# Optimization experiments

Hardware: AMD Instinct MI355X
Metric: run time of the kernel (lower is better)

## Reference

```python
import jax, jax.numpy as jnp
import numpy as np

N, D, H = 4096, 1024, 8
DH = D // H
EPS = 1e-5


def layer_norm(x, g, b):
    mu = jnp.mean(x, axis=-1, keepdims=True)
    var = jnp.mean(jnp.square(x - mu), axis=-1, keepdims=True)
    return (x - mu) * jax.lax.rsqrt(var + EPS) * g + b


def setup_inputs() -> dict:
    key = jax.random.key(0)
    ks = jax.random.split(key, 12)
    s = 0.02
    inp = {
        "x": jax.random.normal(ks[0], (N, D), dtype=jnp.float32),
        "adj": (jax.random.uniform(ks[1], (N, N)) < 0.01).astype(jnp.float32),
        "Wq": jax.random.normal(ks[2], (D, D), dtype=jnp.float32) * s,
        "Wk": jax.random.normal(ks[3], (D, D), dtype=jnp.float32) * s,
        "Wv": jax.random.normal(ks[4], (D, D), dtype=jnp.float32) * s,
        "Wo_w": jax.random.normal(ks[5], (D, D), dtype=jnp.float32) * s,
        "Wo_b": jnp.zeros((D,), dtype=jnp.float32),
        "adj_bias": jnp.full((H,), 1.0, dtype=jnp.float32),
        "ln1_g": jnp.ones((D,), dtype=jnp.float32),
        "ln1_b": jnp.zeros((D,), dtype=jnp.float32),
        "ffn_ln_g": jnp.ones((D,), dtype=jnp.float32),
        "ffn_ln_b": jnp.zeros((D,), dtype=jnp.float32),
        "ffn_w1": jax.random.normal(ks[6], (D, 2 * D), dtype=jnp.float32) * s,
        "ffn_b1": jnp.zeros((2 * D,), dtype=jnp.float32),
        "ffn_w2": jax.random.normal(ks[7], (2 * D, D), dtype=jnp.float32) * s,
        "ffn_b2": jnp.zeros((D,), dtype=jnp.float32),
    }
    return inp


def reference(x, adj, Wq, Wk, Wv, Wo_w, Wo_b, adj_bias, ln1_g, ln1_b,
              ffn_ln_g, ffn_ln_b, ffn_w1, ffn_b1, ffn_w2, ffn_b2):
    scale = DH ** -0.5
    Q = (x @ Wq).reshape(N, H, DH)
    K = (x @ Wk).reshape(N, H, DH)
    V = (x @ Wv).reshape(N, H, DH)
    # attn[i,h,j] = <Q_i, K_j> * scale + beta_h * adj[i,j]
    attn = jnp.einsum('bhd,nhd->bhn', Q, K) * scale
    attn = attn + adj_bias[None, :, None] * adj[:, None, :]
    attn = jax.nn.softmax(attn, axis=-1)  # dropout in eval mode -> identity
    out = jnp.einsum('bhn,nhd->bhd', attn, V).reshape(N, D)
    out = out @ Wo_w + Wo_b
    h = layer_norm(x + out, ln1_g, ln1_b)
    f = layer_norm(h, ffn_ln_g, ffn_ln_b)
    f = jax.nn.gelu(f @ ffn_w1 + ffn_b1, approximate=False) @ ffn_w2 + ffn_b2
    return h + f
```

## Files before the change

### kernel.cpp

```cpp
#include <hip/hip_runtime.h>
#include <hip/hip_bf16.h>
#include <cstdint>
#include <cstddef>

typedef __hip_bfloat16 bf16;
typedef __attribute__((ext_vector_type(8))) short short8;
typedef __attribute__((ext_vector_type(4))) short short4v;
typedef __attribute__((ext_vector_type(4))) float floatx4;
typedef unsigned long long u64;

#define DEVI static __device__ __forceinline__

DEVI void load_lds16(const void* g, void* l) {
  __builtin_amdgcn_global_load_lds((const __attribute__((address_space(1))) unsigned int*)g,
                                   (__attribute__((address_space(3))) unsigned int*)l, 16, 0, 0);
}
DEVI short8 ld8(const bf16* p) { return *(const short8*)p; }
DEVI floatx4 mfma16(short8 a, short8 b, floatx4 c) {
  return __builtin_amdgcn_mfma_f32_16x16x32_bf16(a, b, c, 0, 0, 0);
}
DEVI floatx4 mfma1k(short4v a, short4v b, floatx4 c) {
  return __builtin_amdgcn_mfma_f32_16x16x16bf16_1k(a, b, c, 0, 0, 0);
}
DEVI short bfb(float f) { bf16 h = __float2bfloat16(f); return __builtin_bit_cast(short, h); }
DEVI float fbf(short s) { bf16 h = __builtin_bit_cast(bf16, s); return __bfloat162float(h); }

DEVI void tr_tile(const float* in, bf16* out, int R, int C, int bx, int by) {
  __shared__ float t[32][33];
  int c0 = bx * 32, r0 = by * 32;
  int tx = threadIdx.x & 31, ty = threadIdx.x >> 5;
#pragma unroll
  for (int i = 0; i < 32; i += 8) t[ty + i][tx] = in[(size_t)(r0 + ty + i) * C + c0 + tx];
  __syncthreads();
#pragma unroll
  for (int i = 0; i < 32; i += 8)
    out[(size_t)(c0 + ty + i) * R + r0 + tx] = __float2bfloat16(t[tx][ty + i]);
}

__global__ __launch_bounds__(256)
void prep_all(const float* __restrict__ x, bf16* __restrict__ xb,
              const float* __restrict__ adj, u64* __restrict__ bits,
              const float* Wq, const float* Wk, const float* Wv, const float* Wo,
              const float* W1, const float* W2,
              bf16* Wqkvt, bf16* Wot, bf16* W1t, bf16* W2t) {
  int id = blockIdx.x;
  if (id < 4096) {
    const int row = id, tid = threadIdx.x;
    const int wave = tid >> 6, lane = tid & 63;
    float4 v = ((const float4*)(x + (size_t)row * 1024))[tid];
    bf16* o = xb + (size_t)row * 1024 + tid * 4;
    o[0] = __float2bfloat16(v.x); o[1] = __float2bfloat16(v.y);
    o[2] = __float2bfloat16(v.z); o[3] = __float2bfloat16(v.w);
    const float* arow = adj + (size_t)row * 4096;
#pragma unroll
    for (int it = 0; it < 16; it++) {
      int col = it * 256 + tid;
      u64 m = __ballot(arow[col] != 0.f);
      if (lane == 0) bits[(size_t)row * 64 + it * 4 + wave] = m;
    }
  } else if (id < 8192) {
    int q = id - 4096, w = q >> 10, t = q & 1023;
    const float* in = w == 0 ? Wq : w == 1 ? Wk : w == 2 ? Wv : Wo;
    bf16* out = w == 0 ? Wqkvt : w == 1 ? Wqkvt + 1024ull * 1024
              : w == 2 ? Wqkvt + 2048ull * 1024 : Wot;
    tr_tile(in, out, 1024, 1024, t & 31, t >> 5);
  } else if (id < 10240) {
    int t = id - 8192;
    tr_tile(W1, W1t, 1024, 2048, t & 63, t >> 6);
  } else {
    int t = id - 10240;
    tr_tile(W2, W2t, 2048, 1024, t & 31, t >> 5);
  }
}

__global__ __launch_bounds__(256)
void tr_bf16t(const bf16* __restrict__ in, bf16* __restrict__ out, int inLd) {
  __shared__ bf16 t[32][33];
  int c0 = blockIdx.x * 32, r0 = blockIdx.y * 32;
  int tx = threadIdx.x, ty = threadIdx.y;
#pragma unroll
  for (int i = 0; i < 32; i += 8) t[ty + i][tx] = in[(size_t)(r0 + ty + i) * inLd + c0 + tx];
  __syncthreads();
#pragma unroll
  for (int i = 0; i < 32; i += 8)
    out[(size_t)(c0 + ty + i) * 4096 + r0 + tx] = t[tx][ty + i];
}

template <int MODE, int BN>
__global__ __launch_bounds__(256)
void gemm_bt(const bf16* __restrict__ A, const bf16* __restrict__ Bt,
             const float* __restrict__ bias, const float* __restrict__ resid,
             float* __restrict__ outF, bf16* __restrict__ outB,
             int M, int Nn, int K) {
  constexpr int NI = BN / 32;
  __shared__ alignas(16) bf16 As[3][128 * 32];
  __shared__ alignas(16) bf16 Bs[3][BN * 32];
  const int tid = threadIdx.x;
  const int wave = tid >> 6, lane = tid & 63;
  const int m0 = blockIdx.y * 128, n0 = blockIdx.x * BN;
  const int wr = (wave >> 1) * 64, wc = (wave & 1) * (BN / 2);
  const int l15 = lane & 15, qq = lane >> 4;
  const int lr = lane >> 2, l4 = lane & 3;
  const int T = K >> 5;

  floatx4 acc[4][NI];
#pragma unroll
  for (int i = 0; i < 4; i++)
#pragma unroll
    for (int j = 0; j < NI; j++) acc[i][j] = (floatx4)0.f;

  const bf16* gA0 = A + (size_t)(m0 + wave * 16 + lr) * K + l4 * 8;
  const bf16* gA1 = gA0 + (size_t)64 * K;
  const bf16* gB0 = Bt + (size_t)(n0 + wave * 16 + lr) * K + l4 * 8;
  const bf16* gB1 = gB0 + (size_t)64 * K;
  const int lo = wave * 16 * 32;

  auto stage = [&](int t, int buf) {
    int kt = t * 32;
    load_lds16(gA0 + kt, &As[buf][lo]);
    load_lds16(gA1 + kt, &As[buf][64 * 32 + lo]);
    load_lds16(gB0 + kt, &Bs[buf][lo]);
    if (BN == 128) load_lds16(gB1 + kt, &Bs[buf][64 * 32 + lo]);
  };
  stage(0, 0);
  stage(1, 1);

  int bc = 0;
  for (int t = 0; t < T; ++t) {
    if (t < T - 1) {
      if constexpr (BN == 128)
        asm volatile("s_waitcnt vmcnt(4) lgkmcnt(0)" ::: "memory");
      else
        asm volatile("s_waitcnt vmcnt(3) lgkmcnt(0)" ::: "memory");
    } else {
      asm volatile("s_waitcnt vmcnt(0) lgkmcnt(0)" ::: "memory");
    }
    __builtin_amdgcn_s_barrier();
    if (t + 2 < T) { int bs = bc == 0 ? 2 : bc - 1; stage(t + 2, bs); }

    short8 af[4], bfr[NI];
#pragma unroll
    for (int mi = 0; mi < 4; mi++) af[mi] = ld8(&As[bc][(wr + mi * 16 + l15) * 32 + qq * 8]);
#pragma unroll
    for (int ni = 0; ni < NI; ni++) bfr[ni] = ld8(&Bs[bc][(wc + ni * 16 + l15) * 32 + qq * 8]);
#pragma unroll
    for (int mi = 0; mi < 4; mi++)
#pragma unroll
      for (int ni = 0; ni < NI; ni++)
        acc[mi][ni] = mfma16(af[mi], bfr[ni], acc[mi][ni]);
    bc = bc == 2 ? 0 : bc + 1;
  }

#pragma unroll
  for (int mi = 0; mi < 4; mi++) {
    int row = m0 + wr + mi * 16 + qq * 4;
#pragma unroll
    for (int ni = 0; ni < NI; ni++) {
      int col = n0 + wc + ni * 16 + l15;
      float bv = (MODE >= 1) ? bias[col] : 0.f;
#pragma unroll
      for (int r = 0; r < 4; r++) {
        float v = acc[mi][ni][r] + bv;
        size_t off = (size_t)(row + r) * Nn + col;
        if (MODE == 0) {
          outB[off] = __float2bfloat16(v);
        } else if (MODE == 2) {
          outB[off] = __float2bfloat16(0.5f * v * (1.f + erff(v * 0.70710678118654752f)));
        } else if (MODE == 1) {
          outF[off] = v;
        } else {
          outF[off] = v + resid[off];
        }
      }
    }
  }
}

__global__ __launch_bounds__(256, 2)
void attn_kernel(const bf16* __restrict__ QKV, const bf16* __restrict__ Vt,
                 const u64* __restrict__ adjbits, const float* __restrict__ adj_bias,
                 bf16* __restrict__ AOpart, float* __restrict__ lpart) {
  __shared__ alignas(16) bf16 Kf[16 * 512];
  __shared__ alignas(16) bf16 Vf[16 * 512];
  const int q0 = blockIdx.x * 128;
  const int h = blockIdx.y;
  const int split = blockIdx.z;
  const int k0 = split * 1024;
  const int tid = threadIdx.x, wave = tid >> 6, lane = tid & 63;
  const int l15 = lane & 15, qq = lane >> 4;
  const float beta = adj_bias[h];
  const float scale = 0.08838834764831845f;

  short8 qf[2][4];
#pragma unroll
  for (int mi = 0; mi < 2; mi++)
#pragma unroll
    for (int kk = 0; kk < 4; kk++)
      qf[mi][kk] = ld8(&QKV[(size_t)(q0 + wave * 32 + mi * 16 + l15) * 3072 +
                            h * 128 + kk * 32 + qq * 8]);

  floatx4 o[2][8];
#pragma unroll
  for (int mi = 0; mi < 2; mi++)
#pragma unroll
    for (int d = 0; d < 8; d++) o[mi][d] = (floatx4)0.f;
  float lrow[2] = {0.f, 0.f};

  const size_t abase = (size_t)(q0 + wave * 32 + l15) * 64 + split * 16;

  for (int t = 0; t < 16; t++) {
    const int kt = k0 + t * 64;
    __syncthreads();
#pragma unroll
    for (int i = 0; i < 4; i++) {
      int fi = wave * 4 + i;
      int ni = fi >> 2, kk = fi & 3;
      load_lds16(&QKV[(size_t)(kt + ni * 16 + l15) * 3072 + 1024 + h * 128 + kk * 32 + qq * 8],
                 (char*)Kf + fi * 1024);
      int d = fi >> 1, k2 = fi & 1;
      load_lds16(&Vt[(size_t)(h * 128 + d * 16 + l15) * 4096 + kt + k2 * 32 + qq * 8],
                 (char*)Vf + fi * 1024);
    }
    u64 ab0 = adjbits[abase + t];
    u64 ab1 = adjbits[abase + 1024 + t];
    asm volatile("s_waitcnt vmcnt(0)" ::: "memory");
    __syncthreads();

#pragma unroll
    for (int ni = 0; ni < 4; ni++) {
      floatx4 s0 = (floatx4)0.f, s1 = (floatx4)0.f;
#pragma unroll
      for (int kk = 0; kk < 4; kk++) {
        short8 kf = ld8(&Kf[(ni * 4 + kk) * 512 + lane * 8]);
        s0 = mfma16(kf, qf[0][kk], s0);
        s1 = mfma16(kf, qf[1][kk], s1);
      }
      short4v pa0, pa1;
      {
        float p0, p1, p2, p3;
        int bp = ni * 16 + qq * 4;
        p0 = __expf(fmaf(s0[0], scale, ((ab0 >> (bp + 0)) & 1) ? beta : 0.f));
        p1 = __expf(fmaf(s0[1], scale, ((ab0 >> (bp + 1)) & 1) ? beta : 0.f));
        p2 = __expf(fmaf(s0[2], scale, ((ab0 >> (bp + 2)) & 1) ? beta : 0.f));
        p3 = __expf(fmaf(s0[3], scale, ((ab0 >> (bp + 3)) & 1) ? beta : 0.f));
        lrow[0] += (p0 + p1) + (p2 + p3);
        pa0.x = bfb(p0); pa0.y = bfb(p1); pa0.z = bfb(p2); pa0.w = bfb(p3);
        p0 = __expf(fmaf(s1[0], scale, ((ab1 >> (bp + 0)) & 1) ? beta : 0.f));
        p1 = __expf(fmaf(s1[1], scale, ((ab1 >> (bp + 1)) & 1) ? beta : 0.f));
        p2 = __expf(fmaf(s1[2], scale, ((ab1 >> (bp + 2)) & 1) ? beta : 0.f));
        p3 = __expf(fmaf(s1[3], scale, ((ab1 >> (bp + 3)) & 1) ? beta : 0.f));
        lrow[1] += (p0 + p1) + (p2 + p3);
        pa1.x = bfb(p0); pa1.y = bfb(p1); pa1.z = bfb(p2); pa1.w = bfb(p3);
      }
      const int voff = ((ni & 1) * 2 + (qq >> 1)) * 256 + l15 * 16 + (qq & 1) * 8;
#pragma unroll
      for (int d = 0; d < 8; d++) {
        short4v vf = *(const short4v*)((const char*)Vf + (d * 2 + (ni >> 1)) * 1024 + voff);
        o[0][d] = mfma1k(pa0, vf, o[0][d]);
        o[1][d] = mfma1k(pa1, vf, o[1][d]);
      }
    }
  }

#pragma unroll
  for (int mi = 0; mi < 2; mi++) {
    float v = lrow[mi];
    v += __shfl_xor(v, 16, 64);
    v += __shfl_xor(v, 32, 64);
    if (qq == 0) lpart[((size_t)split * 4096 + q0 + wave * 32 + mi * 16 + l15) * 8 + h] = v;
#pragma unroll
    for (int r = 0; r < 4; r++) {
      int grow = q0 + wave * 32 + mi * 16 + qq * 4 + r;
      bf16* dst = AOpart + ((size_t)split * 4096 + grow) * 1024 + h * 128;
#pragma unroll
      for (int d = 0; d < 8; d++) dst[d * 16 + l15] = __float2bfloat16(o[mi][d][r]);
    }
  }
}

__global__ __launch_bounds__(256)
void attn_norm(const bf16* __restrict__ AOpart, const float* __restrict__ lpart,
               bf16* __restrict__ AO) {
  int row = blockIdx.x, tid = threadIdx.x;
  int h = tid >> 5;
  float ls = 0.f;
#pragma unroll
  for (int s = 0; s < 4; s++) ls += lpart[((size_t)s * 4096 + row) * 8 + h];
  float a0 = 0.f, a1 = 0.f, a2 = 0.f, a3 = 0.f;
#pragma unroll
  for (int s = 0; s < 4; s++) {
    short4v v = *(const short4v*)&AOpart[((size_t)s * 4096 + row) * 1024 + tid * 4];
    a0 += fbf(v.x); a1 += fbf(v.y); a2 += fbf(v.z); a3 += fbf(v.w);
  }
  float inv = 1.f / ls;
  bf16* op = AO + (size_t)row * 1024 + tid * 4;
  op[0] = __float2bfloat16(a0 * inv);
  op[1] = __float2bfloat16(a1 * inv);
  op[2] = __float2bfloat16(a2 * inv);
  op[3] = __float2bfloat16(a3 * inv);
}

DEVI void block_sum2(float& a, float& b, float* red) {
#pragma unroll
  for (int o = 1; o < 64; o <<= 1) { a += __shfl_xor(a, o, 64); b += __shfl_xor(b, o, 64); }
  int wv = threadIdx.x >> 6;
  if ((threadIdx.x & 63) == 0) { red[wv] = a; red[4 + wv] = b; }
  __syncthreads();
  a = red[0] + red[1] + red[2] + red[3];
  b = red[4] + red[5] + red[6] + red[7];
  __syncthreads();
}

__global__ __launch_bounds__(256)
void ln2_kernel(const float* __restrict__ x, const float* __restrict__ ao,
                const float* __restrict__ g1, const float* __restrict__ b1,
                const float* __restrict__ g2, const float* __restrict__ b2,
                float* __restrict__ hout, bf16* __restrict__ fln) {
  __shared__ float red[8];
  const int row = blockIdx.x, tid = threadIdx.x;
  float4 xv = ((const float4*)(x + (size_t)row * 1024))[tid];
  float4 av = ((const float4*)(ao + (size_t)row * 1024))[tid];
  float s0 = xv.x + av.x, s1 = xv.y + av.y, s2 = xv.z + av.z, s3 = xv.w + av.w;
  float sum = s0 + s1 + s2 + s3;
  float ssq = s0 * s0 + s1 * s1 + s2 * s2 + s3 * s3;
  block_sum2(sum, ssq, red);
  float mu = sum * (1.f / 1024.f);
  float rs = rsqrtf(ssq * (1.f / 1024.f) - mu * mu + 1e-5f);
  float4 gv = ((const float4*)g1)[tid], bv = ((const float4*)b1)[tid];
  float h0 = (s0 - mu) * rs * gv.x + bv.x;
  float h1 = (s1 - mu) * rs * gv.y + bv.y;
  float h2 = (s2 - mu) * rs * gv.z + bv.z;
  float h3 = (s3 - mu) * rs * gv.w + bv.w;
  float4 hv; hv.x = h0; hv.y = h1; hv.z = h2; hv.w = h3;
  ((float4*)(hout + (size_t)row * 1024))[tid] = hv;
  float sum2 = h0 + h1 + h2 + h3;
  float ssq2 = h0 * h0 + h1 * h1 + h2 * h2 + h3 * h3;
  block_sum2(sum2, ssq2, red);
  float mu2 = sum2 * (1.f / 1024.f);
  float rs2 = rsqrtf(ssq2 * (1.f / 1024.f) - mu2 * mu2 + 1e-5f);
  float4 g2v = ((const float4*)g2)[tid], b2v = ((const float4*)b2)[tid];
  bf16* op = fln + (size_t)row * 1024 + tid * 4;
  op[0] = __float2bfloat16((h0 - mu2) * rs2 * g2v.x + b2v.x);
  op[1] = __float2bfloat16((h1 - mu2) * rs2 * g2v.y + b2v.y);
  op[2] = __float2bfloat16((h2 - mu2) * rs2 * g2v.z + b2v.z);
  op[3] = __float2bfloat16((h3 - mu2) * rs2 * g2v.w + b2v.w);
}

extern "C" void kernel_launch(void* const* d_in, const int* in_sizes, int n_in,
                              void* d_out, int out_size, void* d_ws, size_t ws_size,
                              hipStream_t stream) {
  const float* x    = (const float*)d_in[0];
  const float* adj  = (const float*)d_in[1];
  const float* Wq   = (const float*)d_in[2];
  const float* Wk   = (const float*)d_in[3];
  const float* Wv   = (const float*)d_in[4];
  const float* Wo   = (const float*)d_in[5];
  const float* Wob  = (const float*)d_in[6];
  const float* adjb = (const float*)d_in[7];
  const float* g1   = (const float*)d_in[8];
  const float* b1   = (const float*)d_in[9];
  const float* g2   = (const float*)d_in[10];
  const float* b2   = (const float*)d_in[11];
  const float* W1   = (const float*)d_in[12];
  const float* fb1  = (const float*)d_in[13];
  const float* W2   = (const float*)d_in[14];
  const float* fb2  = (const float*)d_in[15];
  float* out = (float*)d_out;

  char* w = (char*)d_ws;
  size_t off = 0;
  auto take = [&](size_t bytes) {
    char* p = w + off;
    off += (bytes + 255) & ~(size_t)255;
    return p;
  };
  bf16* xb    = (bf16*)take(4096ull * 1024 * 2);
  bf16* Wqkvt = (bf16*)take(3072ull * 1024 * 2);
  bf16* Wot   = (bf16*)take(1024ull * 1024 * 2);
  bf16* W1t   = (bf16*)take(2048ull * 1024 * 2);
  bf16* W2t   = (bf16*)take(1024ull * 2048 * 2);
  bf16* QKV   = (bf16*)take(4096ull * 3072 * 2);
  bf16* Vt    = (bf16*)take(1024ull * 4096 * 2);
  bf16* AO    = (bf16*)take(4096ull * 1024 * 2);
  u64*  adjbits = (u64*)take(4096ull * 64 * 8);
  float* lpart  = (float*)take(4ull * 4096 * 8 * 4);
  char* big = take(32ull << 20);
  bf16*  AOpart = (bf16*)big;
  float* WoP    = (float*)big;
  float* H   = (float*)take(4096ull * 1024 * 4);
  bf16*  FLN = (bf16*)take(4096ull * 1024 * 2);
  bf16*  G   = (bf16*)take(4096ull * 2048 * 2);

  dim3 tb(32, 8);
  prep_all<<<12288, 256, 0, stream>>>(x, xb, adj, adjbits, Wq, Wk, Wv, Wo, W1, W2,
                                      Wqkvt, Wot, W1t, W2t);
  gemm_bt<0, 128><<<dim3(24, 32), 256, 0, stream>>>(xb, Wqkvt, nullptr, nullptr,
                                                    nullptr, QKV, 4096, 3072, 1024);
  tr_bf16t<<<dim3(32, 128), tb, 0, stream>>>(QKV + 2048, Vt, 3072);
  attn_kernel<<<dim3(32, 8, 4), 256, 0, stream>>>(QKV, Vt, adjbits, adjb, AOpart, lpart);
  attn_norm<<<4096, 256, 0, stream>>>(AOpart, lpart, AO);
  gemm_bt<1, 64><<<dim3(16, 32), 256, 0, stream>>>(AO, Wot, Wob, nullptr,
                                                   WoP, nullptr, 4096, 1024, 1024);
  ln2_kernel<<<4096, 256, 0, stream>>>(x, WoP, g1, b1, g2, b2, H, FLN);
  gemm_bt<2, 128><<<dim3(16, 32), 256, 0, stream>>>(FLN, W1t, fb1, nullptr,
                                                    nullptr, G, 4096, 2048, 1024);
  gemm_bt<3, 64><<<dim3(16, 32), 256, 0, stream>>>(G, W2t, fb2, H,
                                                   out, nullptr, 4096, 1024, 2048);
}
```

Baseline: 432.9 us.

## Double-buffer K/V LDS tiles in attention and use exp2 with prescaled constants

The attention kernel now keeps two LDS buffers for the K and V tiles. It prefetches tile t+1 and the next adjacency bit-words while computing on tile t, so global load latency is no longer exposed every iteration. The softmax exponent folds log2(e) into the scale and bias and calls the hardware exp2 directly. Adjacency bits are extracted from 32-bit halves instead of 64-bit shifts. The explicit vmcnt wait was removed, so correctness relies on the compiler inserting waits for the LDS DMA. LDS use per block doubles, which could limit occupancy.

```diff
diff --git a/kernel.cpp b/kernel.cpp
--- a/kernel.cpp
+++ b/kernel.cpp
@@ -180,16 +180,17 @@
 void attn_kernel(const bf16* __restrict__ QKV, const bf16* __restrict__ Vt,
                  const u64* __restrict__ adjbits, const float* __restrict__ adj_bias,
                  bf16* __restrict__ AOpart, float* __restrict__ lpart) {
-  __shared__ alignas(16) bf16 Kf[16 * 512];
-  __shared__ alignas(16) bf16 Vf[16 * 512];
+  __shared__ alignas(16) bf16 Kf[2][16 * 512];
+  __shared__ alignas(16) bf16 Vf[2][16 * 512];
   const int q0 = blockIdx.x * 128;
   const int h = blockIdx.y;
   const int split = blockIdx.z;
   const int k0 = split * 1024;
   const int tid = threadIdx.x, wave = tid >> 6, lane = tid & 63;
   const int l15 = lane & 15, qq = lane >> 4;
-  const float beta = adj_bias[h];
-  const float scale = 0.08838834764831845f;
+  const float log2e = 1.4426950408889634f;
+  const float beta2 = adj_bias[h] * log2e;
+  const float scale2 = 0.08838834764831845f * log2e;
 
   short8 qf[2][4];
 #pragma unroll
@@ -208,58 +209,72 @@
 
   const size_t abase = (size_t)(q0 + wave * 32 + l15) * 64 + split * 16;
 
-  for (int t = 0; t < 16; t++) {
+  auto stage = [&](int t, int buf) {
     const int kt = k0 + t * 64;
-    __syncthreads();
 #pragma unroll
     for (int i = 0; i < 4; i++) {
       int fi = wave * 4 + i;
       int ni = fi >> 2, kk = fi & 3;
       load_lds16(&QKV[(size_t)(kt + ni * 16 + l15) * 3072 + 1024 + h * 128 + kk * 32 + qq * 8],
-                 (char*)Kf + fi * 1024);
+                 (char*)Kf[buf] + fi * 1024);
       int d = fi >> 1, k2 = fi & 1;
       load_lds16(&Vt[(size_t)(h * 128 + d * 16 + l15) * 4096 + kt + k2 * 32 + qq * 8],
-                 (char*)Vf + fi * 1024);
-    }
-    u64 ab0 = adjbits[abase + t];
-    u64 ab1 = adjbits[abase + 1024 + t];
-    asm volatile("s_waitcnt vmcnt(0)" ::: "memory");
+                 (char*)Vf[buf] + fi * 1024);
+    }
+  };
+
+  stage(0, 0);
+  u64 a0c = adjbits[abase];
+  u64 a1c = adjbits[abase + 1024];
+
+  for (int t = 0; t < 16; t++) {
     __syncthreads();
+    if (t < 15) stage(t + 1, (t + 1) & 1);
+    u64 a0n = 0, a1n = 0;
+    if (t < 15) { a0n = adjbits[abase + t + 1]; a1n = adjbits[abase + 1024 + t + 1]; }
+
+    const bf16* Kc = Kf[t & 1];
+    const bf16* Vc = Vf[t & 1];
+    const uint32_t w0lo = (uint32_t)a0c, w0hi = (uint32_t)(a0c >> 32);
+    const uint32_t w1lo = (uint32_t)a1c, w1hi = (uint32_t)(a1c >> 32);
 
 #pragma unroll
     for (int ni = 0; ni < 4; ni++) {
       floatx4 s0 = (floatx4)0.f, s1 = (floatx4)0.f;
 #pragma unroll
       for (int kk = 0; kk < 4; kk++) {
-        short8 kf = ld8(&Kf[(ni * 4 + kk) * 512 + lane * 8]);
-        s0 = mfma16(kf, qf[0][kk], s0);
-        s1 = mfma16(kf, qf[1][kk], s1);
+        short8 kfr = ld8(&Kc[(ni * 4 + kk) * 512 + lane * 8]);
+        s0 = mfma16(kfr, qf[0][kk], s0);
+        s1 = mfma16(kfr, qf[1][kk], s1);
       }
       short4v pa0, pa1;
       {
+        const uint32_t u0 = (ni >= 2 ? w0hi : w0lo) >> ((ni & 1) * 16);
+        const uint32_t u1 = (ni >= 2 ? w1hi : w1lo) >> ((ni & 1) * 16);
+        const int bp = qq * 4;
         float p0, p1, p2, p3;
-        int bp = ni * 16 + qq * 4;
-        p0 = __expf(fmaf(s0[0], scale, ((ab0 >> (bp + 0)) & 1) ? beta : 0.f));
-        p1 = __expf(fmaf(s0[1], scale, ((ab0 >> (bp + 1)) & 1) ? beta : 0.f));
-        p2 = __expf(fmaf(s0[2], scale, ((ab0 >> (bp + 2)) & 1) ? beta : 0.f));
-        p3 = __expf(fmaf(s0[3], scale, ((ab0 >> (bp + 3)) & 1) ? beta : 0.f));
+        p0 = __builtin_amdgcn_exp2f(fmaf(s0[0], scale2, ((u0 >> (bp + 0)) & 1) ? beta2 : 0.f));
+        p1 = __builtin_amdgcn_exp2f(fmaf(s0[1], scale2, ((u0 >> (bp + 1)) & 1) ? beta2 : 0.f));
+        p2 = __builtin_amdgcn_exp2f(fmaf(s0[2], scale2, ((u0 >> (bp + 2)) & 1) ? beta2 : 0.f));
+        p3 = __builtin_amdgcn_exp2f(fmaf(s0[3], scale2, ((u0 >> (bp + 3)) & 1) ? beta2 : 0.f));
         lrow[0] += (p0 + p1) + (p2 + p3);
         pa0.x = bfb(p0); pa0.y = bfb(p1); pa0.z = bfb(p2); pa0.w = bfb(p3);
-        p0 = __expf(fmaf(s1[0], scale, ((ab1 >> (bp + 0)) & 1) ? beta : 0.f));
-        p1 = __expf(fmaf(s1[1], scale, ((ab1 >> (bp + 1)) & 1) ? beta : 0.f));
-        p2 = __expf(fmaf(s1[2], scale, ((ab1 >> (bp + 2)) & 1) ? beta : 0.f));
-        p3 = __expf(fmaf(s1[3], scale, ((ab1 >> (bp + 3)) & 1) ? beta : 0.f));
+        p0 = __builtin_amdgcn_exp2f(fmaf(s1[0], scale2, ((u1 >> (bp + 0)) & 1) ? beta2 : 0.f));
+        p1 = __builtin_amdgcn_exp2f(fmaf(s1[1], scale2, ((u1 >> (bp + 1)) & 1) ? beta2 : 0.f));
+        p2 = __builtin_amdgcn_exp2f(fmaf(s1[2], scale2, ((u1 >> (bp + 2)) & 1) ? beta2 : 0.f));
+        p3 = __builtin_amdgcn_exp2f(fmaf(s1[3], scale2, ((u1 >> (bp + 3)) & 1) ? beta2 : 0.f));
         lrow[1] += (p0 + p1) + (p2 + p3);
         pa1.x = bfb(p0); pa1.y = bfb(p1); pa1.z = bfb(p2); pa1.w = bfb(p3);
       }
       const int voff = ((ni & 1) * 2 + (qq >> 1)) * 256 + l15 * 16 + (qq & 1) * 8;
 #pragma unroll
       for (int d = 0; d < 8; d++) {
-        short4v vf = *(const short4v*)((const char*)Vf + (d * 2 + (ni >> 1)) * 1024 + voff);
+        short4v vf = *(const short4v*)((const char*)Vc + (d * 2 + (ni >> 1)) * 1024 + voff);
         o[0][d] = mfma1k(pa0, vf, o[0][d]);
         o[1][d] = mfma1k(pa1, vf, o[1][d]);
       }
     }
+    a0c = a0n; a1c = a1n;
   }
 
 #pragma unroll
```

Result: no change. 431.0 us (-0.5%).
